# Kernel tuning notes

Measured on AMD Instinct MI355X. Metric: run time of the kernel, lower is better.

Reference implementation:

```python
import jax, jax.numpy as jnp
import numpy as np

E = 1024      # embed_dim
H = 16        # n_heads
B = 8         # number of varlen segments
LQ = 512      # query tokens per segment (uniform packing)
LKV = 1024    # kv tokens per segment (uniform packing)


def setup_inputs() -> dict:
    key = jax.random.key(0)
    k0, k1, k2, k3 = jax.random.split(key, 4)
    inputs = jax.random.normal(k0, (B * LKV, E), dtype=jnp.float32)
    queries = jax.random.normal(k1, (B * LQ, E), dtype=jnp.float32)
    # cu_seqlens: prefix sums of segment lengths (uniform segments here)
    cu_seqlens_inputs = jnp.arange(B + 1, dtype=jnp.int32) * LKV
    cu_seqlens_queries = jnp.arange(B + 1, dtype=jnp.int32) * LQ
    # nn.MultiheadAttention parameters
    scale = 0.02
    w_in = jax.random.normal(k2, (3 * E, E), dtype=jnp.float32) * scale
    b_in = jnp.zeros((3 * E,), dtype=jnp.float32)
    w_out = jax.random.normal(k3, (E, E), dtype=jnp.float32) * scale
    b_out = jnp.zeros((E,), dtype=jnp.float32)
    return {
        "inputs": inputs,
        "queries": queries,
        "w_in": w_in,
        "b_in": b_in,
        "w_out": w_out,
        "b_out": b_out,
        "cu_seqlens_inputs": cu_seqlens_inputs,
        "cu_seqlens_queries": cu_seqlens_queries,
    }


def reference(inputs, queries, w_in, b_in, w_out, b_out,
              cu_seqlens_inputs, cu_seqlens_queries):
    # Packed varlen cross-attention. Segments are uniform (as produced by
    # setup_inputs), so the ragged computation is expressed as a single
    # batched attention: reshape packed tokens to [B, L, E]. Attention is
    # confined within each segment, matching the original per-segment loop.
    e = inputs.shape[-1]
    dh = e // H
    b = cu_seqlens_inputs.shape[0] - 1
    lkv = inputs.shape[0] // b
    lq = queries.shape[0] // b

    # in_proj: torch computes x @ W.T + b with W = in_proj_weight rows [q;k;v]
    q = queries @ w_in[:e].T + b_in[:e]
    k = inputs @ w_in[e:2 * e].T + b_in[e:2 * e]
    v = inputs @ w_in[2 * e:].T + b_in[2 * e:]

    q = q.reshape(b, lq, H, dh)
    k = k.reshape(b, lkv, H, dh)
    v = v.reshape(b, lkv, H, dh)

    scale = 1.0 / jnp.sqrt(jnp.asarray(dh, q.dtype))
    scores = jnp.einsum('bqhd,bkhd->bhqk', q, k) * scale   # [B,H,Lq,Lkv]
    probs = jax.nn.softmax(scores, axis=-1)
    o = jnp.einsum('bhqk,bkhd->bqhd', probs, v).reshape(b * lq, e)
    return o @ w_out.T + b_out
```

## Files before the change

kernel.cpp:

```cpp
#include <hip/hip_runtime.h>

#define E_DIM 1024
#define NH 16
#define DH 64
#define BSEG 8
#define LQ 512
#define LKV 1024

typedef short bf16x8 __attribute__((ext_vector_type(8)));
typedef float f32x4 __attribute__((ext_vector_type(4)));
typedef unsigned short u16;

__device__ __forceinline__ u16 f2bf(float x) {
    unsigned u = __float_as_uint(x);
    u += 0x7FFF + ((u >> 16) & 1);
    return (u16)(u >> 16);
}

__device__ __forceinline__ void async16(const void* g, const void* l) {
    __builtin_amdgcn_global_load_lds(
        (const __attribute__((address_space(1))) unsigned int*)g,
        (__attribute__((address_space(3))) unsigned int*)l, 16, 0, 0);
}

__global__ __launch_bounds__(256) void cvt_all_kernel(
    const float* __restrict__ inputs, const float* __restrict__ queries,
    const float* __restrict__ w_in, const float* __restrict__ w_out,
    u16* __restrict__ ib, u16* __restrict__ qb,
    u16* __restrict__ wib, u16* __restrict__ wob)
{
    int blk = blockIdx.x;
    const float* s; u16* d; int base;
    if (blk < 8192)        { s = inputs;  d = ib;  base = blk; }
    else if (blk < 12288)  { s = queries; d = qb;  base = blk - 8192; }
    else if (blk < 15360)  { s = w_in;    d = wib; base = blk - 12288; }
    else                   { s = w_out;   d = wob; base = blk - 15360; }
    int i = base * 256 + threadIdx.x;
    float4 v = ((const float4*)s)[i];
    ushort4 o;
    o.x = f2bf(v.x); o.y = f2bf(v.y); o.z = f2bf(v.z); o.w = f2bf(v.w);
    ((ushort4*)d)[i] = o;
}

__global__ __launch_bounds__(256) void proj_gemm_kernel(
    const u16* __restrict__ inputs_b, const u16* __restrict__ queries_b,
    const u16* __restrict__ w_in_b, const float* __restrict__ b_in,
    u16* __restrict__ Kf, u16* __restrict__ Qf, u16* __restrict__ Vf)
{
    __shared__ u16 As[128 * 32];
    __shared__ u16 Ws[128 * 32];

    const int bid = blockIdx.x;
    const bool isQ = (bid >= 1024);
    const int x = bid & 7;
    int bx, by;
    if (!isQ) { int i = bid >> 3;          bx = i >> 3; by = x * 8 + (i & 7); }
    else      { int i = (bid - 1024) >> 3; bx = i >> 2; by = x * 4 + (i & 3); }

    const u16* A = isQ ? queries_b : inputs_b;
    const u16* W = w_in_b + (isQ ? 0 : (size_t)E_DIM * E_DIM);
    const float* bias = b_in + (isQ ? 0 : E_DIM);
    const int m_blk = by * 128;
    const int n_blk = bx * 128;
    const int K = E_DIM;

    const int tid = threadIdx.x;
    const int l = tid & 63;
    const int w = tid >> 6;
    const int m0 = (w & 1) * 64;
    const int n0 = (w >> 1) * 64;
    const int quad = l >> 4;
    const int c = l & 15;

    f32x4 acc[4][4];
    #pragma unroll
    for (int i = 0; i < 4; ++i)
        #pragma unroll
        for (int j = 0; j < 4; ++j)
            acc[i][j] = (f32x4){0.f, 0.f, 0.f, 0.f};

    const int srow = l >> 2;
    const int skoff = (l & 3) * 8;
    const u16* Ag1 = A + (size_t)(m_blk + w * 16 + srow) * K + skoff;
    const u16* Ag2 = A + (size_t)(m_blk + (w + 4) * 16 + srow) * K + skoff;
    const u16* Wg1 = W + (size_t)(n_blk + w * 16 + srow) * K + skoff;
    const u16* Wg2 = W + (size_t)(n_blk + (w + 4) * 16 + srow) * K + skoff;

    for (int k0 = 0; k0 < K; k0 += 32) {
        __syncthreads();
        async16(Ag1 + k0, As + (size_t)w * 512);
        async16(Ag2 + k0, As + (size_t)(w + 4) * 512);
        async16(Wg1 + k0, Ws + (size_t)w * 512);
        async16(Wg2 + k0, Ws + (size_t)(w + 4) * 512);
        __syncthreads();

        bf16x8 af[4], wf[4];
        #pragma unroll
        for (int t = 0; t < 4; ++t) {
            af[t] = *(const bf16x8*)&As[(m0 + t * 16 + c) * 32 + quad * 8];
            wf[t] = *(const bf16x8*)&Ws[(n0 + t * 16 + c) * 32 + quad * 8];
        }
        #pragma unroll
        for (int i = 0; i < 4; ++i)
            #pragma unroll
            for (int j = 0; j < 4; ++j)
                acc[i][j] = __builtin_amdgcn_mfma_f32_16x16x32_bf16(
                    af[i], wf[j], acc[i][j], 0, 0, 0);
    }

    #pragma unroll
    for (int jj = 0; jj < 4; ++jj) {
        int col = n_blk + n0 + jj * 16 + c;
        float bv = bias[col];
        if (isQ || col < 1024) {
            u16* dst = isQ ? Qf : Kf;
            int hh = col >> 6, d = col & 63;
            int dq = d >> 3, dj = d & 7;
            #pragma unroll
            for (int i = 0; i < 4; ++i) {
                int t = (m_blk + m0 + i * 16) >> 4;
                size_t base = ((size_t)(t * NH + hh)) * 1024
                            + (size_t)(dq * 16 + quad * 4) * 8 + dj;
                #pragma unroll
                for (int r = 0; r < 4; ++r)
                    dst[base + (size_t)r * 8] = f2bf(acc[i][jj][r] + bv);
            }
        } else {
            int vcol = col - 1024;
            int hv = vcol >> 6, d = vcol & 63;
            int td = d >> 4, ct = d & 15;
            #pragma unroll
            for (int i = 0; i < 4; ++i) {
                int tok = m_blk + m0 + i * 16;
                int g32 = tok >> 5;
                int jo = (tok & 16) >> 2;
                ushort4 pk;
                pk.x = f2bf(acc[i][jj][0] + bv);
                pk.y = f2bf(acc[i][jj][1] + bv);
                pk.z = f2bf(acc[i][jj][2] + bv);
                pk.w = f2bf(acc[i][jj][3] + bv);
                *(ushort4*)(Vf + ((size_t)(g32 * NH + hv)) * 2048
                            + (size_t)((td * 4 + quad) * 16 + ct) * 8 + jo) = pk;
            }
        }
    }
}

struct KVfrags { bf16x8 kf[4][2]; bf16x8 vf[2][4]; };

__global__ __launch_bounds__(256) void attn_kernel(
    const u16* __restrict__ Qf, const u16* __restrict__ Kf,
    const u16* __restrict__ Vf, u16* __restrict__ Ob)
{
    const int tid = threadIdx.x;
    const int l = tid & 63;
    const int w = tid >> 6;
    const int quad = l >> 4;
    const int c = l & 15;
    const int bid = blockIdx.x;
    const int h = bid & 15;
    const int b = (bid >> 4) & 7;
    const int qt = bid >> 7;
    const int q0 = b * LQ + qt * 64 + w * 16;
    const float C1 = 0.18033688011112042f;

    bf16x8 qf[2];
    {
        size_t qb = ((size_t)((q0 >> 4) * NH + h)) * 1024 + (size_t)l * 8;
        qf[0] = *(const bf16x8*)(Qf + qb);
        qf[1] = *(const bf16x8*)(Qf + qb + 512);
    }

    f32x4 o[4];
    #pragma unroll
    for (int td = 0; td < 4; ++td) o[td] = (f32x4){0.f, 0.f, 0.f, 0.f};
    float m_i = -1e30f, l_i = 0.f;

    auto load_kv = [&](int kv0, KVfrags& dst) {
        const int kvg = b * LKV + kv0;
        #pragma unroll
        for (int nt = 0; nt < 4; ++nt) {
            size_t kb = ((size_t)((((kvg >> 4) + nt) * NH) + h)) * 1024 + (size_t)l * 8;
            dst.kf[nt][0] = *(const bf16x8*)(Kf + kb);
            dst.kf[nt][1] = *(const bf16x8*)(Kf + kb + 512);
        }
        #pragma unroll
        for (int g = 0; g < 2; ++g) {
            size_t vb = ((size_t)((((kvg >> 5) + g) * NH) + h)) * 2048 + (size_t)l * 8;
            #pragma unroll
            for (int td = 0; td < 4; ++td)
                dst.vf[g][td] = *(const bf16x8*)(Vf + vb + td * 512);
        }
    };

    auto step = [&](KVfrags& cv) {
        f32x4 s[4];
        #pragma unroll
        for (int nt = 0; nt < 4; ++nt) s[nt] = (f32x4){0.f, 0.f, 0.f, 0.f};
        #pragma unroll
        for (int nt = 0; nt < 4; ++nt)
            #pragma unroll
            for (int hk = 0; hk < 2; ++hk)
                s[nt] = __builtin_amdgcn_mfma_f32_16x16x32_bf16(
                    cv.kf[nt][hk], qf[hk], s[nt], 0, 0, 0);

        float vm = -1e30f;
        #pragma unroll
        for (int nt = 0; nt < 4; ++nt)
            #pragma unroll
            for (int r = 0; r < 4; ++r) vm = fmaxf(vm, s[nt][r]);
        vm = fmaxf(vm, __shfl_xor(vm, 16, 64));
        vm = fmaxf(vm, __shfl_xor(vm, 32, 64));
        float mnew = fmaxf(m_i, vm);
        float alpha = __builtin_amdgcn_exp2f((m_i - mnew) * C1);
        m_i = mnew;

        float p[4][4];
        float rs = 0.f;
        #pragma unroll
        for (int nt = 0; nt < 4; ++nt)
            #pragma unroll
            for (int r = 0; r < 4; ++r) {
                p[nt][r] = __builtin_amdgcn_exp2f((s[nt][r] - mnew) * C1);
                rs += p[nt][r];
            }
        rs += __shfl_xor(rs, 16, 64);
        rs += __shfl_xor(rs, 32, 64);
        l_i = l_i * alpha + rs;

        float ar[4];
        #pragma unroll
        for (int r = 0; r < 4; ++r) ar[r] = __shfl(alpha, quad * 4 + r, 16);
        #pragma unroll
        for (int td = 0; td < 4; ++td)
            #pragma unroll
            for (int r = 0; r < 4; ++r) o[td][r] *= ar[r];

        bf16x8 af[2];
        #pragma unroll
        for (int g = 0; g < 2; ++g)
            #pragma unroll
            for (int r = 0; r < 4; ++r) {
                af[g][r]     = (short)f2bf(p[2 * g][r]);
                af[g][4 + r] = (short)f2bf(p[2 * g + 1][r]);
            }

        #pragma unroll
        for (int g = 0; g < 2; ++g)
            #pragma unroll
            for (int td = 0; td < 4; ++td)
                o[td] = __builtin_amdgcn_mfma_f32_16x16x32_bf16(
                    af[g], cv.vf[g][td], o[td], 0, 0, 0);
    };

    KVfrags bufA, bufB;
    load_kv(0, bufA);
    #pragma unroll
    for (int it = 0; it < 16; it += 2) {
        if (it + 1 < 16) load_kv((it + 1) * 64, bufB);
        step(bufA);
        if (it + 2 < 16) load_kv((it + 2) * 64, bufA);
        if (it + 1 < 16) step(bufB);
    }

    float invl = 1.f / l_i;
    float ir[4];
    #pragma unroll
    for (int r = 0; r < 4; ++r) ir[r] = __shfl(invl, quad * 4 + r, 16);
    #pragma unroll
    for (int td = 0; td < 4; ++td)
        #pragma unroll
        for (int r = 0; r < 4; ++r)
            Ob[(size_t)(q0 + quad * 4 + r) * E_DIM + h * 64 + td * 16 + c] =
                f2bf(o[td][r] * ir[r]);
}

__global__ __launch_bounds__(256) void out_gemm_kernel(
    const u16* __restrict__ A, const u16* __restrict__ W,
    const float* __restrict__ bias, float* __restrict__ Cf)
{
    __shared__ u16 As[128 * 32];
    __shared__ u16 Ws[128 * 32];

    const int K = E_DIM, N = E_DIM;
    const int bid = blockIdx.x;
    const int x = bid & 7;
    const int i_ = bid >> 3;
    const int m_blk = (x * 4 + (i_ & 3)) * 128;
    const int n_blk = (i_ >> 2) * 128;

    const int tid = threadIdx.x;
    const int l = tid & 63;
    const int w = tid >> 6;
    const int m0 = (w & 1) * 64;
    const int n0 = (w >> 1) * 64;
    const int quad = l >> 4;
    const int c = l & 15;

    f32x4 acc[4][4];
    #pragma unroll
    for (int i = 0; i < 4; ++i)
        #pragma unroll
        for (int j = 0; j < 4; ++j)
            acc[i][j] = (f32x4){0.f, 0.f, 0.f, 0.f};

    const int srow = l >> 2;
    const int skoff = (l & 3) * 8;
    const u16* Ag1 = A + (size_t)(m_blk + w * 16 + srow) * K + skoff;
    const u16* Ag2 = A + (size_t)(m_blk + (w + 4) * 16 + srow) * K + skoff;
    const u16* Wg1 = W + (size_t)(n_blk + w * 16 + srow) * K + skoff;
    const u16* Wg2 = W + (size_t)(n_blk + (w + 4) * 16 + srow) * K + skoff;

    for (int k0 = 0; k0 < K; k0 += 32) {
        __syncthreads();
        async16(Ag1 + k0, As + (size_t)w * 512);
        async16(Ag2 + k0, As + (size_t)(w + 4) * 512);
        async16(Wg1 + k0, Ws + (size_t)w * 512);
        async16(Wg2 + k0, Ws + (size_t)(w + 4) * 512);
        __syncthreads();

        bf16x8 af[4], wf[4];
        #pragma unroll
        for (int t = 0; t < 4; ++t) {
            af[t] = *(const bf16x8*)&As[(m0 + t * 16 + c) * 32 + quad * 8];
            wf[t] = *(const bf16x8*)&Ws[(n0 + t * 16 + c) * 32 + quad * 8];
        }
        #pragma unroll
        for (int i = 0; i < 4; ++i)
            #pragma unroll
            for (int j = 0; j < 4; ++j)
                acc[i][j] = __builtin_amdgcn_mfma_f32_16x16x32_bf16(
                    af[i], wf[j], acc[i][j], 0, 0, 0);
    }

    #pragma unroll
    for (int j = 0; j < 4; ++j) {
        int col = n_blk + n0 + j * 16 + c;
        float bv = bias[col];
        #pragma unroll
        for (int i = 0; i < 4; ++i) {
            int row = m_blk + m0 + i * 16 + quad * 4;
            #pragma unroll
            for (int r = 0; r < 4; ++r)
                Cf[(size_t)(row + r) * N + col] = acc[i][j][r] + bv;
        }
    }
}

extern "C" void kernel_launch(void* const* d_in, const int* in_sizes, int n_in,
                              void* d_out, int out_size, void* d_ws, size_t ws_size,
                              hipStream_t stream) {
    const float* inputs  = (const float*)d_in[0];
    const float* queries = (const float*)d_in[1];
    const float* w_in    = (const float*)d_in[2];
    const float* b_in    = (const float*)d_in[3];
    const float* w_out   = (const float*)d_in[4];
    const float* b_out   = (const float*)d_in[5];
    float* out = (float*)d_out;

    const int NQ = BSEG * LQ;
    const int NKV = BSEG * LKV;

    u16* inputs_b  = (u16*)d_ws;
    u16* queries_b = inputs_b  + (size_t)NKV * E_DIM;
    u16* w_in_b    = queries_b + (size_t)NQ * E_DIM;
    u16* w_out_b   = w_in_b    + (size_t)3 * E_DIM * E_DIM;
    u16* Qf        = w_out_b   + (size_t)E_DIM * E_DIM;
    u16* Kf        = Qf        + (size_t)NQ * E_DIM;
    u16* Vf        = Kf        + (size_t)NKV * E_DIM;
    u16* Ob        = Vf        + (size_t)NKV * E_DIM;

    dim3 blk(256);

    cvt_all_kernel<<<16384, blk, 0, stream>>>(
        inputs, queries, w_in, w_out, inputs_b, queries_b, w_in_b, w_out_b);

    proj_gemm_kernel<<<1280, blk, 0, stream>>>(
        inputs_b, queries_b, w_in_b, b_in, Kf, Qf, Vf);

    attn_kernel<<<1024, blk, 0, stream>>>(Qf, Kf, Vf, Ob);

    out_gemm_kernel<<<256, blk, 0, stream>>>(
        Ob, w_out_b, b_out, out);
}
```

Baseline: 241.1 us.

## Double-buffer LDS in projection GEMMs and vectorize epilogue stores via transposed MFMA

Both the input-projection and output-projection GEMMs now use two LDS buffers, so the async global-to-LDS copy of the next K slice is issued before the current slice is computed. This removes one barrier per iteration and hides load latency behind the MFMAs. The MFMA operands are also swapped for the Q/K and output paths so each lane holds four consecutive columns, which lets the epilogue write packed ushort4 or float4 values and read the bias as a float4 instead of issuing scalar stores. LDS use doubles, which may lower occupancy, and the V path keeps the old operand order and epilogue.

```diff
diff --git a/kernel.cpp b/kernel.cpp
--- a/kernel.cpp
+++ b/kernel.cpp
@@ -47,8 +47,8 @@
     const u16* __restrict__ w_in_b, const float* __restrict__ b_in,
     u16* __restrict__ Kf, u16* __restrict__ Qf, u16* __restrict__ Vf)
 {
-    __shared__ u16 As[128 * 32];
-    __shared__ u16 Ws[128 * 32];
+    __shared__ u16 As[2][128 * 32];
+    __shared__ u16 Ws[2][128 * 32];
 
     const int bid = blockIdx.x;
     const bool isQ = (bid >= 1024);
@@ -56,6 +56,8 @@
     int bx, by;
     if (!isQ) { int i = bid >> 3;          bx = i >> 3; by = x * 8 + (i & 7); }
     else      { int i = (bid - 1024) >> 3; bx = i >> 2; by = x * 4 + (i & 3); }
+
+    const bool isV = (!isQ) && (bx >= 8);
 
     const u16* A = isQ ? queries_b : inputs_b;
     const u16* W = w_in_b + (isQ ? 0 : (size_t)E_DIM * E_DIM);
@@ -86,46 +88,70 @@
     const u16* Wg1 = W + (size_t)(n_blk + w * 16 + srow) * K + skoff;
     const u16* Wg2 = W + (size_t)(n_blk + (w + 4) * 16 + srow) * K + skoff;
 
+    auto stage = [&](int b, int k0) {
+        async16(Ag1 + k0, As[b] + (size_t)w * 512);
+        async16(Ag2 + k0, As[b] + (size_t)(w + 4) * 512);
+        async16(Wg1 + k0, Ws[b] + (size_t)w * 512);
+        async16(Wg2 + k0, Ws[b] + (size_t)(w + 4) * 512);
+    };
+
+    stage(0, 0);
+    __syncthreads();
+
+    int cur = 0;
     for (int k0 = 0; k0 < K; k0 += 32) {
+        if (k0 + 32 < K) stage(cur ^ 1, k0 + 32);
+
+        bf16x8 af[4], wf[4];
+        #pragma unroll
+        for (int t = 0; t < 4; ++t) {
+            af[t] = *(const bf16x8*)&As[cur][(m0 + t * 16 + c) * 32 + quad * 8];
+            wf[t] = *(const bf16x8*)&Ws[cur][(n0 + t * 16 + c) * 32 + quad * 8];
+        }
+        if (isV) {
+            #pragma unroll
+            for (int i = 0; i < 4; ++i)
+                #pragma unroll
+                for (int j = 0; j < 4; ++j)
+                    acc[i][j] = __builtin_amdgcn_mfma_f32_16x16x32_bf16(
+                        af[i], wf[j], acc[i][j], 0, 0, 0);
+        } else {
+            #pragma unroll
+            for (int i = 0; i < 4; ++i)
+                #pragma unroll
+                for (int j = 0; j < 4; ++j)
+                    acc[i][j] = __builtin_amdgcn_mfma_f32_16x16x32_bf16(
+                        wf[j], af[i], acc[i][j], 0, 0, 0);
+        }
         __syncthreads();
-        async16(Ag1 + k0, As + (size_t)w * 512);
-        async16(Ag2 + k0, As + (size_t)(w + 4) * 512);
-        async16(Wg1 + k0, Ws + (size_t)w * 512);
-        async16(Wg2 + k0, Ws + (size_t)(w + 4) * 512);
-        __syncthreads();
-
-        bf16x8 af[4], wf[4];
-        #pragma unroll
-        for (int t = 0; t < 4; ++t) {
-            af[t] = *(const bf16x8*)&As[(m0 + t * 16 + c) * 32 + quad * 8];
-            wf[t] = *(const bf16x8*)&Ws[(n0 + t * 16 + c) * 32 + quad * 8];
-        }
-        #pragma unroll
-        for (int i = 0; i < 4; ++i)
-            #pragma unroll
-            for (int j = 0; j < 4; ++j)
-                acc[i][j] = __builtin_amdgcn_mfma_f32_16x16x32_bf16(
-                    af[i], wf[j], acc[i][j], 0, 0, 0);
-    }
-
-    #pragma unroll
-    for (int jj = 0; jj < 4; ++jj) {
-        int col = n_blk + n0 + jj * 16 + c;
-        float bv = bias[col];
-        if (isQ || col < 1024) {
-            u16* dst = isQ ? Qf : Kf;
-            int hh = col >> 6, d = col & 63;
-            int dq = d >> 3, dj = d & 7;
+        cur ^= 1;
+    }
+
+    if (!isV) {
+        u16* dst = isQ ? Qf : Kf;
+        #pragma unroll
+        for (int jj = 0; jj < 4; ++jj) {
+            const int colb = n_blk + n0 + jj * 16 + quad * 4;
+            const float4 bv = *(const float4*)&bias[colb];
+            const int hh = colb >> 6;
+            const int d  = colb & 63;
+            const size_t doff = (size_t)(d >> 3) * 128 + (size_t)c * 8 + (d & 7);
             #pragma unroll
             for (int i = 0; i < 4; ++i) {
-                int t = (m_blk + m0 + i * 16) >> 4;
-                size_t base = ((size_t)(t * NH + hh)) * 1024
-                            + (size_t)(dq * 16 + quad * 4) * 8 + dj;
-                #pragma unroll
-                for (int r = 0; r < 4; ++r)
-                    dst[base + (size_t)r * 8] = f2bf(acc[i][jj][r] + bv);
+                const int t16 = ((m_blk + m0) >> 4) + i;
+                ushort4 pk;
+                pk.x = f2bf(acc[i][jj][0] + bv.x);
+                pk.y = f2bf(acc[i][jj][1] + bv.y);
+                pk.z = f2bf(acc[i][jj][2] + bv.z);
+                pk.w = f2bf(acc[i][jj][3] + bv.w);
+                *(ushort4*)(dst + ((size_t)(t16 * NH + hh)) * 1024 + doff) = pk;
             }
-        } else {
+        }
+    } else {
+        #pragma unroll
+        for (int jj = 0; jj < 4; ++jj) {
+            int col = n_blk + n0 + jj * 16 + c;
+            float bv = bias[col];
             int vcol = col - 1024;
             int hv = vcol >> 6, d = vcol & 63;
             int td = d >> 4, ct = d & 15;
@@ -279,8 +305,8 @@
     const u16* __restrict__ A, const u16* __restrict__ W,
     const float* __restrict__ bias, float* __restrict__ Cf)
 {
-    __shared__ u16 As[128 * 32];
-    __shared__ u16 Ws[128 * 32];
+    __shared__ u16 As[2][128 * 32];
+    __shared__ u16 Ws[2][128 * 32];
 
     const int K = E_DIM, N = E_DIM;
     const int bid = blockIdx.x;
@@ -311,38 +337,49 @@
     const u16* Wg1 = W + (size_t)(n_blk + w * 16 + srow) * K + skoff;
     const u16* Wg2 = W + (size_t)(n_blk + (w + 4) * 16 + srow) * K + skoff;
 
+    auto stage = [&](int b, int k0) {
+        async16(Ag1 + k0, As[b] + (size_t)w * 512);
+        async16(Ag2 + k0, As[b] + (size_t)(w + 4) * 512);
+        async16(Wg1 + k0, Ws[b] + (size_t)w * 512);
+        async16(Wg2 + k0, Ws[b] + (size_t)(w + 4) * 512);
+    };
+
+    stage(0, 0);
+    __syncthreads();
+
+    int cur = 0;
     for (int k0 = 0; k0 < K; k0 += 32) {
-        __syncthreads();
-        async16(Ag1 + k0, As + (size_t)w * 512);
-        async16(Ag2 + k0, As + (size_t)(w + 4) * 512);
-        async16(Wg1 + k0, Ws + (size_t)w * 512);
-        async16(Wg2 + k0, Ws + (size_t)(w + 4) * 512);
-        __syncthreads();
+        if (k0 + 32 < K) stage(cur ^ 1, k0 + 32);
 
         bf16x8 af[4], wf[4];
         #pragma unroll
         for (int t = 0; t < 4; ++t) {
-            af[t] = *(const bf16x8*)&As[(m0 + t * 16 + c) * 32 + quad * 8];
-            wf[t] = *(const bf16x8*)&Ws[(n0 + t * 16 + c) * 32 + quad * 8];
+            af[t] = *(const bf16x8*)&As[cur][(m0 + t * 16 + c) * 32 + quad * 8];
+            wf[t] = *(const bf16x8*)&Ws[cur][(n0 + t * 16 + c) * 32 + quad * 8];
         }
         #pragma unroll
         for (int i = 0; i < 4; ++i)
             #pragma unroll
             for (int j = 0; j < 4; ++j)
                 acc[i][j] = __builtin_amdgcn_mfma_f32_16x16x32_bf16(
-                    af[i], wf[j], acc[i][j], 0, 0, 0);
+                    wf[j], af[i], acc[i][j], 0, 0, 0);
+        __syncthreads();
+        cur ^= 1;
     }
 
     #pragma unroll
     for (int j = 0; j < 4; ++j) {
-        int col = n_blk + n0 + j * 16 + c;
-        float bv = bias[col];
+        const int colb = n_blk + n0 + j * 16 + quad * 4;
+        const float4 bv = *(const float4*)&bias[colb];
         #pragma unroll
         for (int i = 0; i < 4; ++i) {
-            int row = m_blk + m0 + i * 16 + quad * 4;
-            #pragma unroll
-            for (int r = 0; r < 4; ++r)
-                Cf[(size_t)(row + r) * N + col] = acc[i][j][r] + bv;
+            const int row = m_blk + m0 + i * 16 + c;
+            float4 o4;
+            o4.x = acc[i][j][0] + bv.x;
+            o4.y = acc[i][j][1] + bv.y;
+            o4.z = acc[i][j][2] + bv.z;
+            o4.w = acc[i][j][3] + bv.w;
+            *(float4*)&Cf[(size_t)row * N + colb] = o4;
         }
     }
 }
```

Result: slower. 265.5 us (+10.1%).

## Double K-step per barrier in GEMMs and vectorize output GEMM stores

Applied to the files above, without the earlier changes.

Both projection and output GEMMs now load a 64-wide K slab (two 32-wide halves in separate LDS buffers) per pair of barriers, halving the number of sync points per K loop. The output GEMM swaps MFMA operand order so each lane holds four consecutive columns, enabling float4 bias loads and float4 stores to the fp32 output instead of scalar strided stores. Occupancy hint of 5 blocks is added to the projection kernel. LDS use doubles per block, which may reduce occupancy.

```diff
diff --git a/kernel.cpp b/kernel.cpp
--- a/kernel.cpp
+++ b/kernel.cpp
@@ -42,13 +42,13 @@
     ((ushort4*)d)[i] = o;
 }
 
-__global__ __launch_bounds__(256) void proj_gemm_kernel(
+__global__ __launch_bounds__(256, 5) void proj_gemm_kernel(
     const u16* __restrict__ inputs_b, const u16* __restrict__ queries_b,
     const u16* __restrict__ w_in_b, const float* __restrict__ b_in,
     u16* __restrict__ Kf, u16* __restrict__ Qf, u16* __restrict__ Vf)
 {
-    __shared__ u16 As[128 * 32];
-    __shared__ u16 Ws[128 * 32];
+    __shared__ u16 As[2][128 * 32];
+    __shared__ u16 Ws[2][128 * 32];
 
     const int bid = blockIdx.x;
     const bool isQ = (bid >= 1024);
@@ -81,31 +81,37 @@
 
     const int srow = l >> 2;
     const int skoff = (l & 3) * 8;
-    const u16* Ag1 = A + (size_t)(m_blk + w * 16 + srow) * K + skoff;
-    const u16* Ag2 = A + (size_t)(m_blk + (w + 4) * 16 + srow) * K + skoff;
-    const u16* Wg1 = W + (size_t)(n_blk + w * 16 + srow) * K + skoff;
-    const u16* Wg2 = W + (size_t)(n_blk + (w + 4) * 16 + srow) * K + skoff;
-
-    for (int k0 = 0; k0 < K; k0 += 32) {
+    const u16* Ag = A + (size_t)(m_blk + w * 32 + srow) * K + skoff;
+    const u16* Wg = W + (size_t)(n_blk + w * 32 + srow) * K + skoff;
+
+    for (int k0 = 0; k0 < K; k0 += 64) {
         __syncthreads();
-        async16(Ag1 + k0, As + (size_t)w * 512);
-        async16(Ag2 + k0, As + (size_t)(w + 4) * 512);
-        async16(Wg1 + k0, Ws + (size_t)w * 512);
-        async16(Wg2 + k0, Ws + (size_t)(w + 4) * 512);
+        #pragma unroll
+        for (int hf = 0; hf < 2; ++hf)
+            #pragma unroll
+            for (int t = 0; t < 2; ++t) {
+                const size_t soff = (size_t)t * 16 * K + k0 + hf * 32;
+                const size_t doff = (size_t)(w * 32 + t * 16) * 32;
+                async16(Ag + soff, &As[hf][0] + doff);
+                async16(Wg + soff, &Ws[hf][0] + doff);
+            }
         __syncthreads();
 
-        bf16x8 af[4], wf[4];
-        #pragma unroll
-        for (int t = 0; t < 4; ++t) {
-            af[t] = *(const bf16x8*)&As[(m0 + t * 16 + c) * 32 + quad * 8];
-            wf[t] = *(const bf16x8*)&Ws[(n0 + t * 16 + c) * 32 + quad * 8];
-        }
-        #pragma unroll
-        for (int i = 0; i < 4; ++i)
-            #pragma unroll
-            for (int j = 0; j < 4; ++j)
-                acc[i][j] = __builtin_amdgcn_mfma_f32_16x16x32_bf16(
-                    af[i], wf[j], acc[i][j], 0, 0, 0);
+        #pragma unroll
+        for (int hf = 0; hf < 2; ++hf) {
+            bf16x8 af[4], wf[4];
+            #pragma unroll
+            for (int t = 0; t < 4; ++t) {
+                af[t] = *(const bf16x8*)&As[hf][(m0 + t * 16 + c) * 32 + quad * 8];
+                wf[t] = *(const bf16x8*)&Ws[hf][(n0 + t * 16 + c) * 32 + quad * 8];
+            }
+            #pragma unroll
+            for (int i = 0; i < 4; ++i)
+                #pragma unroll
+                for (int j = 0; j < 4; ++j)
+                    acc[i][j] = __builtin_amdgcn_mfma_f32_16x16x32_bf16(
+                        af[i], wf[j], acc[i][j], 0, 0, 0);
+        }
     }
 
     #pragma unroll
@@ -279,8 +285,8 @@
     const u16* __restrict__ A, const u16* __restrict__ W,
     const float* __restrict__ bias, float* __restrict__ Cf)
 {
-    __shared__ u16 As[128 * 32];
-    __shared__ u16 Ws[128 * 32];
+    __shared__ u16 As[2][128 * 32];
+    __shared__ u16 Ws[2][128 * 32];
 
     const int K = E_DIM, N = E_DIM;
     const int bid = blockIdx.x;
@@ -306,43 +312,52 @@
 
     const int srow = l >> 2;
     const int skoff = (l & 3) * 8;
-    const u16* Ag1 = A + (size_t)(m_blk + w * 16 + srow) * K + skoff;
-    const u16* Ag2 = A + (size_t)(m_blk + (w + 4) * 16 + srow) * K + skoff;
-    const u16* Wg1 = W + (size_t)(n_blk + w * 16 + srow) * K + skoff;
-    const u16* Wg2 = W + (size_t)(n_blk + (w + 4) * 16 + srow) * K + skoff;
-
-    for (int k0 = 0; k0 < K; k0 += 32) {
+    const u16* Ag = A + (size_t)(m_blk + w * 32 + srow) * K + skoff;
+    const u16* Wg = W + (size_t)(n_blk + w * 32 + srow) * K + skoff;
+
+    for (int k0 = 0; k0 < K; k0 += 64) {
         __syncthreads();
-        async16(Ag1 + k0, As + (size_t)w * 512);
-        async16(Ag2 + k0, As + (size_t)(w + 4) * 512);
-        async16(Wg1 + k0, Ws + (size_t)w * 512);
-        async16(Wg2 + k0, Ws + (size_t)(w + 4) * 512);
+        #pragma unroll
+        for (int hf = 0; hf < 2; ++hf)
+            #pragma unroll
+            for (int t = 0; t < 2; ++t) {
+                const size_t soff = (size_t)t * 16 * K + k0 + hf * 32;
+                const size_t doff = (size_t)(w * 32 + t * 16) * 32;
+                async16(Ag + soff, &As[hf][0] + doff);
+                async16(Wg + soff, &Ws[hf][0] + doff);
+            }
         __syncthreads();
 
-        bf16x8 af[4], wf[4];
-        #pragma unroll
-        for (int t = 0; t < 4; ++t) {
-            af[t] = *(const bf16x8*)&As[(m0 + t * 16 + c) * 32 + quad * 8];
-            wf[t] = *(const bf16x8*)&Ws[(n0 + t * 16 + c) * 32 + quad * 8];
-        }
-        #pragma unroll
-        for (int i = 0; i < 4; ++i)
-            #pragma unroll
-            for (int j = 0; j < 4; ++j)
-                acc[i][j] = __builtin_amdgcn_mfma_f32_16x16x32_bf16(
-                    af[i], wf[j], acc[i][j], 0, 0, 0);
+        #pragma unroll
+        for (int hf = 0; hf < 2; ++hf) {
+            bf16x8 af[4], wf[4];
+            #pragma unroll
+            for (int t = 0; t < 4; ++t) {
+                af[t] = *(const bf16x8*)&As[hf][(m0 + t * 16 + c) * 32 + quad * 8];
+                wf[t] = *(const bf16x8*)&Ws[hf][(n0 + t * 16 + c) * 32 + quad * 8];
+            }
+            #pragma unroll
+            for (int i = 0; i < 4; ++i)
+                #pragma unroll
+                for (int j = 0; j < 4; ++j)
+                    acc[i][j] = __builtin_amdgcn_mfma_f32_16x16x32_bf16(
+                        wf[j], af[i], acc[i][j], 0, 0, 0);
+        }
     }
 
     #pragma unroll
     for (int j = 0; j < 4; ++j) {
-        int col = n_blk + n0 + j * 16 + c;
-        float bv = bias[col];
+        const int colb = n_blk + n0 + j * 16 + quad * 4;
+        const float4 bv = *(const float4*)&bias[colb];
         #pragma unroll
         for (int i = 0; i < 4; ++i) {
-            int row = m_blk + m0 + i * 16 + quad * 4;
-            #pragma unroll
-            for (int r = 0; r < 4; ++r)
-                Cf[(size_t)(row + r) * N + col] = acc[i][j][r] + bv;
+            const int row = m_blk + m0 + i * 16 + c;
+            float4 o4;
+            o4.x = acc[i][j][0] + bv.x;
+            o4.y = acc[i][j][1] + bv.y;
+            o4.z = acc[i][j][2] + bv.z;
+            o4.w = acc[i][j][3] + bv.w;
+            *(float4*)&Cf[(size_t)row * N + colb] = o4;
         }
     }
 }
```

Result: faster. 227.8 us (-5.5%).
